# Kernel tuning notes

Hardware: AMD Instinct MI355X
Metric: run time of the kernel (lower is better)

The kernel has to match this reference:

```python
import jax, jax.numpy as jnp
import numpy as np

T, B, E, H = 2048, 2, 1024, 16
HD = E // H
NEG = -1e9  # large negative for causal additive mask


def setup_inputs() -> dict:
    key = jax.random.key(0)
    ks = jax.random.split(key, 6)
    s = 0.02
    query = jax.random.normal(ks[0], (T, B, E), jnp.float32)
    # causal additive mask, as commonly passed to this module's attn_mask arg
    attn_mask = jnp.triu(jnp.full((T, T), NEG, jnp.float32), k=1)
    key_padding_mask = jnp.zeros((B, T), jnp.bool_)
    Wq = jax.random.normal(ks[1], (E, E), jnp.float32) * s
    Wk = jax.random.normal(ks[2], (E, E), jnp.float32) * s
    Wv = jax.random.normal(ks[3], (E, E), jnp.float32) * s
    Wo = jax.random.normal(ks[4], (E, E), jnp.float32) * s
    bq = jnp.zeros((E,), jnp.float32)
    bk = jnp.zeros((E,), jnp.float32)
    bv = jnp.zeros((E,), jnp.float32)
    bo = jnp.zeros((E,), jnp.float32)
    return {"query": query, "attn_mask": attn_mask, "key_padding_mask": key_padding_mask,
            "Wq": Wq, "bq": bq, "Wk": Wk, "bk": bk, "Wv": Wv, "bv": bv, "Wo": Wo, "bo": bo}


def _shape(x):
    # [T, B, E] -> [B*H, T, HD]; E splits as (H, HD), flat index = b*H + h
    return x.reshape(T, B * H, HD).transpose(1, 0, 2)


def reference(query, attn_mask, key_padding_mask, Wq, bq, Wk, bk, Wv, bv, Wo, bo):
    scaling = HD ** -0.5
    q = (query @ Wq.T + bq) * scaling  # scale q as in torch code
    k = query @ Wk.T + bk              # self-attention path (static_kv=False)
    v = query @ Wv.T + bv
    q, k, v = _shape(q), _shape(k), _shape(v)            # [B*H, T, HD]
    w = jnp.einsum('bth,bsh->bts', q, k)                  # [B*H, T, S]
    w = w.reshape(B, H, T, T) + attn_mask                 # additive mask broadcast
    w = jnp.where(key_padding_mask[:, None, None, :], -jnp.inf, w)
    p = jax.nn.softmax(w, axis=-1).reshape(B * H, T, T)   # dropout p=0 (eval)
    o = jnp.einsum('bts,bsh->bth', p, v)                  # [B*H, T, HD]
    o = o.transpose(1, 0, 2).reshape(T, B, E)
    return o @ Wo.T + bo
```

## Files before the change

kernel.cpp:

```cpp
#include <hip/hip_runtime.h>

#define Tt 2048
#define Bb 2
#define Ee 1024
#define Hh 16
#define HD 64
#define BH 32

typedef __attribute__((ext_vector_type(8))) short short8;
typedef __attribute__((ext_vector_type(4))) short short4v;
typedef __attribute__((ext_vector_type(8))) __bf16 bf16x8;
typedef __attribute__((ext_vector_type(4))) float floatx4;

#define OFF_X  0
#define OFF_WQ 4194304
#define OFF_WK 5242880
#define OFF_WV 6291456
#define OFF_WO 7340032
#define OFF_Q  8388608
#define OFF_K  12582912
#define OFF_V  16777216
#define OFF_O  20971520

__device__ __forceinline__ short f2bf(float f) {
  union { float f; unsigned u; } a; a.f = f;
  unsigned r = a.u + 0x7fffu + ((a.u >> 16) & 1u);
  return (short)(r >> 16);
}

__device__ __forceinline__ floatx4 mfma16(short8 a, short8 b, floatx4 c) {
  return __builtin_amdgcn_mfma_f32_16x16x32_bf16(
      __builtin_bit_cast(bf16x8, a), __builtin_bit_cast(bf16x8, b), c, 0, 0, 0);
}

__device__ __forceinline__ floatx4 mfma_k16(short4v a, short4v b, floatx4 c) {
#if __has_builtin(__builtin_amdgcn_mfma_f32_16x16x16bf16_1k)
  return __builtin_amdgcn_mfma_f32_16x16x16bf16_1k(a, b, c, 0, 0, 0);
#else
  floatx4 d;
  asm("v_mfma_f32_16x16x16_bf16 %0, %1, %2, %3" : "=v"(d) : "v"(a), "v"(b), "v"(c));
  return d;
#endif
}

__device__ __forceinline__ void gl_lds16(const short* g, short* l) {
  __builtin_amdgcn_global_load_lds(
      (const __attribute__((address_space(1))) void*)g,
      (__attribute__((address_space(3))) void*)l, 16, 0, 0);
}

__global__ __launch_bounds__(256)
void convert_kernel(const float* __restrict__ x, const float* __restrict__ wq,
                    const float* __restrict__ wk, const float* __restrict__ wv,
                    const float* __restrict__ wo, short* __restrict__ dst)
{
  const int i4 = blockIdx.x * 256 + threadIdx.x;
  const int f = i4 * 4;
  const float* src;
  int local;
  if (f < 4194304) { src = x; local = f; }
  else {
    int gg = f - 4194304;
    int wsel = gg >> 20;
    local = gg & 1048575;
    src = (wsel == 0) ? wq : (wsel == 1) ? wk : (wsel == 2) ? wv : wo;
  }
  floatx4 v = *reinterpret_cast<const floatx4*>(src + local);
  short4 o;
  o.x = f2bf(v[0]); o.y = f2bf(v[1]); o.z = f2bf(v[2]); o.w = f2bf(v[3]);
  *reinterpret_cast<short4*>(dst + f) = o;
}

__global__ __launch_bounds__(256, 2)
void qkv_kernel(short* __restrict__ ws, const float* __restrict__ bq,
                const float* __restrict__ bk, const float* __restrict__ bv)
{
  __shared__ short smem[2][8192];
  const int t = threadIdx.x;
  const int lane = t & 63;
  const int w = t >> 6;
  const int g = lane >> 4, c = lane & 15;
  const int rb = blockIdx.x * 128;
  const int cb = blockIdx.y * 128;
  const int rw = (w >> 1) * 64, cw2 = (w & 1) * 64;

  const short* gA[2]; const short* gB[2]; int oC[2];
#pragma unroll
  for (int i = 0; i < 2; i++) {
    const int cid = t + 256 * i;
    const int row = cid >> 2;
    const int lch = (cid & 3) ^ ((row + (row >> 2)) & 3);
    gA[i] = ws + OFF_X + (rb + row) * 1024 + lch * 8;
    gB[i] = ws + OFF_WQ + (cb + row) * 1024 + lch * 8;
    oC[i] = cid * 8;
  }
  const int xr = (g ^ ((c + (c >> 2)) & 3)) * 8;

  floatx4 acc[4][4];
#pragma unroll
  for (int i = 0; i < 4; i++)
#pragma unroll
    for (int j = 0; j < 4; j++) acc[i][j] = (floatx4){0.f, 0.f, 0.f, 0.f};

#pragma unroll
  for (int i = 0; i < 2; i++) {
    gl_lds16(gA[i], &smem[0][oC[i]]);
    gl_lds16(gB[i], &smem[0][4096 + oC[i]]);
  }
  __syncthreads();

  for (int kt = 0; kt < 32; kt++) {
    const int cur = kt & 1;
    if (kt < 31) {
      const int kn = (kt + 1) * 32;
#pragma unroll
      for (int i = 0; i < 2; i++) {
        gl_lds16(gA[i] + kn, &smem[cur ^ 1][oC[i]]);
        gl_lds16(gB[i] + kn, &smem[cur ^ 1][4096 + oC[i]]);
      }
    }
    short8 af[4], bf[4];
#pragma unroll
    for (int mi = 0; mi < 4; mi++)
      af[mi] = *reinterpret_cast<const short8*>(&smem[cur][(rw + mi * 16 + c) * 32 + xr]);
#pragma unroll
    for (int ni = 0; ni < 4; ni++)
      bf[ni] = *reinterpret_cast<const short8*>(&smem[cur][4096 + (cw2 + ni * 16 + c) * 32 + xr]);
#pragma unroll
    for (int mi = 0; mi < 4; mi++)
#pragma unroll
      for (int ni = 0; ni < 4; ni++)
        acc[mi][ni] = mfma16(af[mi], bf[ni], acc[mi][ni]);
    __syncthreads();
  }

  const int m = cb >> 10;
  const int lcb = cb & 1023;
  if (m < 2) {
#pragma unroll
    for (int ni = 0; ni < 4; ni++) {
      const int lc = lcb + cw2 + ni * 16 + c;
      const int h = lc >> 6, d = lc & 63;
      const float bcol = (m == 0 ? bq : bk)[lc];
#pragma unroll
      for (int mi = 0; mi < 4; mi++)
#pragma unroll
        for (int r = 0; r < 4; r++) {
          const int row = rb + rw + mi * 16 + g * 4 + r;
          const int tt = row >> 1, b = row & 1;
          float v = acc[mi][ni][r] + bcol;
          if (m == 0) v *= 0.18033688f;
          ws[(m == 0 ? OFF_Q : OFF_K) + ((b * Hh + h) * Tt + tt) * HD + d] = f2bf(v);
        }
    }
  } else {
    short* vt = &smem[0][0];
    const int hb = lcb >> 6;
    for (int b = 0; b < 2; b++) {
      __syncthreads();
#pragma unroll
      for (int ni = 0; ni < 4; ni++) {
        const int lcol = cw2 + ni * 16 + c;
        const float bcol = bv[lcb + lcol];
#pragma unroll
        for (int mi = 0; mi < 4; mi++)
#pragma unroll
          for (int rr = 0; rr < 2; rr++) {
            const int r = rr * 2 + b;
            const int rloc = rw + mi * 16 + g * 4 + r;
            vt[lcol * 72 + (rloc >> 1)] = f2bf(acc[mi][ni][r] + bcol);
          }
      }
      __syncthreads();
#pragma unroll
      for (int i = 0; i < 4; i++) {
        const int u = t + 256 * i;
        const int lcol = u >> 3, seg = u & 7;
        short8 vv = *reinterpret_cast<const short8*>(vt + lcol * 72 + seg * 8);
        const int h = hb + (lcol >> 6), d = lcol & 63;
        *reinterpret_cast<short8*>(ws + OFF_V + ((b * Hh + h) * HD + d) * Tt
                                   + (rb >> 1) + seg * 8) = vv;
      }
    }
  }
}

__global__ __launch_bounds__(256, 2)
void gemm_o(const short* __restrict__ ws, const float* __restrict__ bo,
            float* __restrict__ dout)
{
  __shared__ short As[2][128 * 64];
  __shared__ short Bs[2][64 * 64];
  const int t = threadIdx.x;
  const int lane = t & 63;
  const int w = t >> 6;
  const int g = lane >> 4, c = lane & 15;
  const int rb = blockIdx.x * 128, cb = blockIdx.y * 64;
  const int rw = (w >> 1) * 64, cw = (w & 1) * 32;

  const short* gA[4]; int oA[4];
#pragma unroll
  for (int i = 0; i < 4; i++) {
    const int cid = t + 256 * i;
    const int row = cid >> 3;
    const int col8 = (cid & 7) ^ (row & 7);
    gA[i] = ws + OFF_O + (rb + row) * 1024 + col8 * 8;
    oA[i] = cid * 8;
  }
  const short* gB[2]; int oB[2];
#pragma unroll
  for (int i = 0; i < 2; i++) {
    const int cid = t + 256 * i;
    const int row = cid >> 3;
    const int col8 = (cid & 7) ^ (row & 7);
    gB[i] = ws + OFF_WO + (cb + row) * 1024 + col8 * 8;
    oB[i] = cid * 8;
  }
  const int x0 = (g ^ (c & 7)) * 8;

  floatx4 acc[4][2];
#pragma unroll
  for (int i = 0; i < 4; i++)
#pragma unroll
    for (int j = 0; j < 2; j++) acc[i][j] = (floatx4){0.f, 0.f, 0.f, 0.f};

#pragma unroll
  for (int i = 0; i < 4; i++) gl_lds16(gA[i], &As[0][oA[i]]);
#pragma unroll
  for (int i = 0; i < 2; i++) gl_lds16(gB[i], &Bs[0][oB[i]]);
  __syncthreads();

  for (int it = 0; it < 16; it++) {
    const int cur = it & 1;
    if (it < 15) {
      const int kn = (it + 1) * 64;
#pragma unroll
      for (int i = 0; i < 4; i++) gl_lds16(gA[i] + kn, &As[cur ^ 1][oA[i]]);
#pragma unroll
      for (int i = 0; i < 2; i++) gl_lds16(gB[i] + kn, &Bs[cur ^ 1][oB[i]]);
    }
#pragma unroll
    for (int kk = 0; kk < 2; kk++) {
      const int xo = x0 ^ (kk * 32);
      short8 af[4], bfr[2];
#pragma unroll
      for (int mi = 0; mi < 4; mi++)
        af[mi] = *reinterpret_cast<const short8*>(&As[cur][(rw + mi * 16 + c) * 64 + xo]);
#pragma unroll
      for (int ni = 0; ni < 2; ni++)
        bfr[ni] = *reinterpret_cast<const short8*>(&Bs[cur][(cw + ni * 16 + c) * 64 + xo]);
#pragma unroll
      for (int mi = 0; mi < 4; mi++)
#pragma unroll
        for (int ni = 0; ni < 2; ni++)
          acc[mi][ni] = mfma16(af[mi], bfr[ni], acc[mi][ni]);
    }
    __syncthreads();
  }

#pragma unroll
  for (int ni = 0; ni < 2; ni++) {
    const int col = cb + cw + ni * 16 + c;
    const float bcol = bo[col];
#pragma unroll
    for (int mi = 0; mi < 4; mi++)
#pragma unroll
      for (int r = 0; r < 4; r++) {
        const int row = rb + rw + mi * 16 + g * 4 + r;
        dout[row * 1024 + col] = acc[mi][ni][r] + bcol;
      }
  }
}

__global__ __launch_bounds__(256, 3)
void attn_kernel(short* __restrict__ ws, const unsigned char* __restrict__ kpm)
{
  __shared__ __align__(16) char smem[35840];
  short* KV  = reinterpret_cast<short*>(smem);
  float* bufA = reinterpret_cast<float*>(smem);
  float* bufB = reinterpret_cast<float*>(smem + 17408);
  float* Ls   = reinterpret_cast<float*>(smem + 34816);

  const int t = threadIdx.x;
  const int lane = t & 63;
  const int w = t >> 6;
  const int g = lane >> 4, c = lane & 15;
  const int bh = blockIdx.x;
  const int b = bh >> 4;
  const int h = bh & 15;
  const int qt = 31 - (int)blockIdx.y;
  const int qrow0 = qt * 64;

  const short* Qp = ws + OFF_Q + bh * Tt * HD;
  const short* Kp = ws + OFF_K + bh * Tt * HD;
  const short* Vp = ws + OFF_V + bh * HD * Tt;

  const short* gK[2]; const short* gV[2]; int lo[2];
#pragma unroll
  for (int i = 0; i < 2; i++) {
    const int cid = t + 256 * i;
    const int row = cid >> 3;
    const int col8 = (cid & 7) ^ (row & 7);
    gK[i] = Kp + row * HD + col8 * 8;
    gV[i] = Vp + row * Tt + col8 * 8;
    lo[i] = cid * 8;
  }

  short8 qf[4][2];
#pragma unroll
  for (int qs = 0; qs < 4; qs++) {
    const short* qr = Qp + (qrow0 + qs * 16 + c) * HD + g * 8;
    qf[qs][0] = *reinterpret_cast<const short8*>(qr);
    qf[qs][1] = *reinterpret_cast<const short8*>(qr + 32);
  }

  const uint4* kpv = reinterpret_cast<const uint4*>(kpm + b * Tt);
  uint4 k0v = kpv[lane * 2], k1v = kpv[lane * 2 + 1];
  const bool nz = (k0v.x | k0v.y | k0v.z | k0v.w | k1v.x | k1v.y | k1v.z | k1v.w) != 0;
  const unsigned long long kpany = __ballot(nz);

  float lt[4] = {0.f, 0.f, 0.f, 0.f};
  floatx4 acc[4][4];
#pragma unroll
  for (int i = 0; i < 4; i++)
#pragma unroll
    for (int j = 0; j < 4; j++) acc[i][j] = (floatx4){0.f, 0.f, 0.f, 0.f};

  const int ktmax = qt;
#pragma unroll
  for (int i = 0; i < 2; i++) gl_lds16(gK[i], &KV[lo[i]]);
#pragma unroll
  for (int i = 0; i < 2; i++) gl_lds16(gV[i], &KV[8192 + lo[i]]);
  __syncthreads();

  const int krow = w * 16 + c;
  const int kx0 = (g ^ (c & 7)) * 8;
  const int vcol = (((2 * w + (g >> 1)) ^ (c & 7)) * 8) + (g & 1) * 4;

  for (int kt = 0; kt <= ktmax; kt++) {
    const int cur = kt & 1;
    if (kt < ktmax) {
      const int kn = (kt + 1) * 64;
#pragma unroll
      for (int i = 0; i < 2; i++) gl_lds16(gK[i] + kn * HD, &KV[(cur ^ 1) * 4096 + lo[i]]);
#pragma unroll
      for (int i = 0; i < 2; i++) gl_lds16(gV[i] + kn, &KV[8192 + (cur ^ 1) * 4096 + lo[i]]);
    }
    const short* kr = &KV[cur * 4096 + krow * 64];
    const short8 kb0 = *reinterpret_cast<const short8*>(kr + kx0);
    const short8 kb1 = *reinterpret_cast<const short8*>(kr + (kx0 ^ 32));
    floatx4 st[4];
#pragma unroll
    for (int qs = 0; qs < 4; qs++) {
      floatx4 z = (floatx4){0.f, 0.f, 0.f, 0.f};
      z = mfma16(kb0, qf[qs][0], z);
      z = mfma16(kb1, qf[qs][1], z);
      st[qs] = z;
    }
    if ((kpany >> (2 * kt)) & 3ULL) {
#pragma unroll
      for (int r = 0; r < 4; r++)
        if (kpm[b * Tt + kt * 64 + w * 16 + g * 4 + r] != 0) {
#pragma unroll
          for (int qs = 0; qs < 4; qs++) st[qs][r] = -1e30f;
        }
    }
    if (kt == ktmax) {
      const int kl = w * 16 + g * 4;
#pragma unroll
      for (int qs = 0; qs < 4; qs++)
#pragma unroll
        for (int r = 0; r < 4; r++)
          if (kl + r > qs * 16 + c) st[qs][r] = -1e30f;
    }
    short4v pa[4];
#pragma unroll
    for (int qs = 0; qs < 4; qs++) {
      float p0 = __builtin_amdgcn_exp2f(st[qs][0]);
      float p1 = __builtin_amdgcn_exp2f(st[qs][1]);
      float p2 = __builtin_amdgcn_exp2f(st[qs][2]);
      float p3 = __builtin_amdgcn_exp2f(st[qs][3]);
      lt[qs] += (p0 + p1) + (p2 + p3);
      unsigned u0 = __builtin_bit_cast(unsigned, p0) + 0x8000u;
      unsigned u1 = __builtin_bit_cast(unsigned, p1) + 0x8000u;
      unsigned u2 = __builtin_bit_cast(unsigned, p2) + 0x8000u;
      unsigned u3 = __builtin_bit_cast(unsigned, p3) + 0x8000u;
      uint2 pk;
      pk.x = __builtin_amdgcn_perm(u1, u0, 0x07060302u);
      pk.y = __builtin_amdgcn_perm(u3, u2, 0x07060302u);
      pa[qs] = __builtin_bit_cast(short4v, pk);
    }
    const short* vb0 = &KV[8192 + cur * 4096];
    short4v vb[4];
#pragma unroll
    for (int dt = 0; dt < 4; dt++)
      vb[dt] = *reinterpret_cast<const short4v*>(vb0 + (dt * 16 + c) * 64 + vcol);
#pragma unroll
    for (int qs = 0; qs < 4; qs++)
#pragma unroll
      for (int dt = 0; dt < 4; dt++)
        acc[qs][dt] = mfma_k16(pa[qs], vb[dt], acc[qs][dt]);
    __syncthreads();
  }

#pragma unroll
  for (int qs = 0; qs < 4; qs++) {
    lt[qs] += __shfl_xor(lt[qs], 16);
    lt[qs] += __shfl_xor(lt[qs], 32);
  }
  if (g == 0) {
#pragma unroll
    for (int qs = 0; qs < 4; qs++) Ls[w * 64 + qs * 16 + c] = lt[qs];
  }
  float* mybuf = (w < 2) ? bufA : bufB;
  if ((w & 1) == 0) {
#pragma unroll
    for (int qs = 0; qs < 4; qs++)
#pragma unroll
      for (int dt = 0; dt < 4; dt++)
#pragma unroll
        for (int r = 0; r < 4; r++)
          mybuf[(qs * 16 + g * 4 + r) * 68 + dt * 16 + c] = acc[qs][dt][r];
  }
  __syncthreads();
  if (w & 1) {
#pragma unroll
    for (int qs = 0; qs < 4; qs++)
#pragma unroll
      for (int dt = 0; dt < 4; dt++)
#pragma unroll
        for (int r = 0; r < 4; r++)
          mybuf[(qs * 16 + g * 4 + r) * 68 + dt * 16 + c] += acc[qs][dt][r];
  }
  __syncthreads();
  const int row = w * 16 + (lane >> 2);
  const int dseg = (lane & 3) * 16;
  const float inv = 1.f / (Ls[row] + Ls[64 + row] + Ls[128 + row] + Ls[192 + row]);
  short* op = ws + OFF_O + ((qrow0 + row) * Bb + b) * Ee + h * 64 + dseg;
#pragma unroll
  for (int i = 0; i < 2; i++) {
    floatx4 a0 = *reinterpret_cast<const floatx4*>(&bufA[row * 68 + dseg + i * 8]);
    floatx4 a1 = *reinterpret_cast<const floatx4*>(&bufA[row * 68 + dseg + i * 8 + 4]);
    floatx4 b0 = *reinterpret_cast<const floatx4*>(&bufB[row * 68 + dseg + i * 8]);
    floatx4 b1 = *reinterpret_cast<const floatx4*>(&bufB[row * 68 + dseg + i * 8 + 4]);
    short8 s;
#pragma unroll
    for (int j = 0; j < 4; j++) s[j] = f2bf((a0[j] + b0[j]) * inv);
#pragma unroll
    for (int j = 0; j < 4; j++) s[4 + j] = f2bf((a1[j] + b1[j]) * inv);
    *reinterpret_cast<short8*>(op + i * 8) = s;
  }
}

extern "C" void kernel_launch(void* const* d_in, const int* in_sizes, int n_in,
                              void* d_out, int out_size, void* d_ws, size_t ws_size,
                              hipStream_t stream)
{
  const float* query = (const float*)d_in[0];
  const unsigned char* kpm = (const unsigned char*)d_in[2];
  const float* Wq = (const float*)d_in[3];
  const float* bq = (const float*)d_in[4];
  const float* Wk = (const float*)d_in[5];
  const float* bk = (const float*)d_in[6];
  const float* Wv = (const float*)d_in[7];
  const float* bv = (const float*)d_in[8];
  const float* Wo = (const float*)d_in[9];
  const float* bo = (const float*)d_in[10];
  short* ws = (short*)d_ws;
  float* out = (float*)d_out;

  convert_kernel<<<dim3(8192), dim3(256), 0, stream>>>(query, Wq, Wk, Wv, Wo, ws);
  qkv_kernel<<<dim3(32, 24), dim3(256), 0, stream>>>(ws, bq, bk, bv);
  attn_kernel<<<dim3(32, 32), dim3(256), 0, stream>>>(ws, kpm);
  gemm_o<<<dim3(32, 16), dim3(256), 0, stream>>>(ws, bo, out);
}
```

Before: 184.4 us.

## Drop LDS staging in attention, process key tiles in pairs, retile output GEMM

The attention kernel no longer stages K and V through LDS with double buffering. Each wave now reads its K and V fragments straight from global memory and handles two key tiles per iteration, so P·V can use the K=32 MFMA with its __syncthreads removed. The output projection GEMM moves to 128x128 tiles with a K-step of 32 and a new swizzle, and occupancy hints change. This removes LDS traffic and barriers but puts more load on global memory and the cache, and waves no longer share the K and V tiles they fetch.

Measured after the change: 206.0 us. 11.7% more time.

```diff
diff --git a/kernel.cpp b/kernel.cpp
--- a/kernel.cpp
+++ b/kernel.cpp
@@ -47,6 +47,22 @@
   __builtin_amdgcn_global_load_lds(
       (const __attribute__((address_space(1))) void*)g,
       (__attribute__((address_space(3))) void*)l, 16, 0, 0);
+}
+
+__device__ __forceinline__ uint2 exppack(floatx4 s, float& l) {
+  float p0 = __builtin_amdgcn_exp2f(s[0]);
+  float p1 = __builtin_amdgcn_exp2f(s[1]);
+  float p2 = __builtin_amdgcn_exp2f(s[2]);
+  float p3 = __builtin_amdgcn_exp2f(s[3]);
+  l += (p0 + p1) + (p2 + p3);
+  unsigned u0 = __builtin_bit_cast(unsigned, p0) + 0x8000u;
+  unsigned u1 = __builtin_bit_cast(unsigned, p1) + 0x8000u;
+  unsigned u2 = __builtin_bit_cast(unsigned, p2) + 0x8000u;
+  unsigned u3 = __builtin_bit_cast(unsigned, p3) + 0x8000u;
+  uint2 pk;
+  pk.x = __builtin_amdgcn_perm(u1, u0, 0x07060302u);
+  pk.y = __builtin_amdgcn_perm(u3, u2, 0x07060302u);
+  return pk;
 }
 
 __global__ __launch_bounds__(256)
@@ -189,78 +205,68 @@
 void gemm_o(const short* __restrict__ ws, const float* __restrict__ bo,
             float* __restrict__ dout)
 {
-  __shared__ short As[2][128 * 64];
-  __shared__ short Bs[2][64 * 64];
+  __shared__ short smem[2][8192];
   const int t = threadIdx.x;
   const int lane = t & 63;
   const int w = t >> 6;
   const int g = lane >> 4, c = lane & 15;
-  const int rb = blockIdx.x * 128, cb = blockIdx.y * 64;
-  const int rw = (w >> 1) * 64, cw = (w & 1) * 32;
-
-  const short* gA[4]; int oA[4];
-#pragma unroll
-  for (int i = 0; i < 4; i++) {
-    const int cid = t + 256 * i;
-    const int row = cid >> 3;
-    const int col8 = (cid & 7) ^ (row & 7);
-    gA[i] = ws + OFF_O + (rb + row) * 1024 + col8 * 8;
-    oA[i] = cid * 8;
-  }
-  const short* gB[2]; int oB[2];
+  const int rb = blockIdx.x * 128;
+  const int cb = blockIdx.y * 128;
+  const int rw = (w >> 1) * 64, cw2 = (w & 1) * 64;
+
+  const short* gA[2]; const short* gB[2]; int oC[2];
 #pragma unroll
   for (int i = 0; i < 2; i++) {
     const int cid = t + 256 * i;
-    const int row = cid >> 3;
-    const int col8 = (cid & 7) ^ (row & 7);
-    gB[i] = ws + OFF_WO + (cb + row) * 1024 + col8 * 8;
-    oB[i] = cid * 8;
-  }
-  const int x0 = (g ^ (c & 7)) * 8;
-
-  floatx4 acc[4][2];
+    const int row = cid >> 2;
+    const int lch = (cid & 3) ^ ((row + (row >> 2)) & 3);
+    gA[i] = ws + OFF_O + (rb + row) * 1024 + lch * 8;
+    gB[i] = ws + OFF_WO + (cb + row) * 1024 + lch * 8;
+    oC[i] = cid * 8;
+  }
+  const int xr = (g ^ ((c + (c >> 2)) & 3)) * 8;
+
+  floatx4 acc[4][4];
 #pragma unroll
   for (int i = 0; i < 4; i++)
 #pragma unroll
-    for (int j = 0; j < 2; j++) acc[i][j] = (floatx4){0.f, 0.f, 0.f, 0.f};
-
-#pragma unroll
-  for (int i = 0; i < 4; i++) gl_lds16(gA[i], &As[0][oA[i]]);
-#pragma unroll
-  for (int i = 0; i < 2; i++) gl_lds16(gB[i], &Bs[0][oB[i]]);
+    for (int j = 0; j < 4; j++) acc[i][j] = (floatx4){0.f, 0.f, 0.f, 0.f};
+
+#pragma unroll
+  for (int i = 0; i < 2; i++) {
+    gl_lds16(gA[i], &smem[0][oC[i]]);
+    gl_lds16(gB[i], &smem[0][4096 + oC[i]]);
+  }
   __syncthreads();
 
-  for (int it = 0; it < 16; it++) {
-    const int cur = it & 1;
-    if (it < 15) {
-      const int kn = (it + 1) * 64;
-#pragma unroll
-      for (int i = 0; i < 4; i++) gl_lds16(gA[i] + kn, &As[cur ^ 1][oA[i]]);
-#pragma unroll
-      for (int i = 0; i < 2; i++) gl_lds16(gB[i] + kn, &Bs[cur ^ 1][oB[i]]);
-    }
-#pragma unroll
-    for (int kk = 0; kk < 2; kk++) {
-      const int xo = x0 ^ (kk * 32);
-      short8 af[4], bfr[2];
-#pragma unroll
-      for (int mi = 0; mi < 4; mi++)
-        af[mi] = *reinterpret_cast<const short8*>(&As[cur][(rw + mi * 16 + c) * 64 + xo]);
-#pragma unroll
-      for (int ni = 0; ni < 2; ni++)
-        bfr[ni] = *reinterpret_cast<const short8*>(&Bs[cur][(cw + ni * 16 + c) * 64 + xo]);
-#pragma unroll
-      for (int mi = 0; mi < 4; mi++)
-#pragma unroll
-        for (int ni = 0; ni < 2; ni++)
-          acc[mi][ni] = mfma16(af[mi], bfr[ni], acc[mi][ni]);
-    }
+  for (int kt = 0; kt < 32; kt++) {
+    const int cur = kt & 1;
+    if (kt < 31) {
+      const int kn = (kt + 1) * 32;
+#pragma unroll
+      for (int i = 0; i < 2; i++) {
+        gl_lds16(gA[i] + kn, &smem[cur ^ 1][oC[i]]);
+        gl_lds16(gB[i] + kn, &smem[cur ^ 1][4096 + oC[i]]);
+      }
+    }
+    short8 af[4], bf[4];
+#pragma unroll
+    for (int mi = 0; mi < 4; mi++)
+      af[mi] = *reinterpret_cast<const short8*>(&smem[cur][(rw + mi * 16 + c) * 32 + xr]);
+#pragma unroll
+    for (int ni = 0; ni < 4; ni++)
+      bf[ni] = *reinterpret_cast<const short8*>(&smem[cur][4096 + (cw2 + ni * 16 + c) * 32 + xr]);
+#pragma unroll
+    for (int mi = 0; mi < 4; mi++)
+#pragma unroll
+      for (int ni = 0; ni < 4; ni++)
+        acc[mi][ni] = mfma16(af[mi], bf[ni], acc[mi][ni]);
     __syncthreads();
   }
 
 #pragma unroll
-  for (int ni = 0; ni < 2; ni++) {
-    const int col = cb + cw + ni * 16 + c;
+  for (int ni = 0; ni < 4; ni++) {
+    const int col = cb + cw2 + ni * 16 + c;
     const float bcol = bo[col];
 #pragma unroll
     for (int mi = 0; mi < 4; mi++)
@@ -272,11 +278,10 @@
   }
 }
 
-__global__ __launch_bounds__(256, 3)
+__global__ __launch_bounds__(256, 2)
 void attn_kernel(short* __restrict__ ws, const unsigned char* __restrict__ kpm)
 {
   __shared__ __align__(16) char smem[35840];
-  short* KV  = reinterpret_cast<short*>(smem);
   float* bufA = reinterpret_cast<float*>(smem);
   float* bufB = reinterpret_cast<float*>(smem + 17408);
   float* Ls   = reinterpret_cast<float*>(smem + 34816);
@@ -295,17 +300,6 @@
   const short* Kp = ws + OFF_K + bh * Tt * HD;
   const short* Vp = ws + OFF_V + bh * HD * Tt;
 
-  const short* gK[2]; const short* gV[2]; int lo[2];
-#pragma unroll
-  for (int i = 0; i < 2; i++) {
-    const int cid = t + 256 * i;
-    const int row = cid >> 3;
-    const int col8 = (cid & 7) ^ (row & 7);
-    gK[i] = Kp + row * HD + col8 * 8;
-    gV[i] = Vp + row * Tt + col8 * 8;
-    lo[i] = cid * 8;
-  }
-
   short8 qf[4][2];
 #pragma unroll
   for (int qs = 0; qs < 4; qs++) {
@@ -326,46 +320,113 @@
 #pragma unroll
     for (int j = 0; j < 4; j++) acc[i][j] = (floatx4){0.f, 0.f, 0.f, 0.f};
 
-  const int ktmax = qt;
-#pragma unroll
-  for (int i = 0; i < 2; i++) gl_lds16(gK[i], &KV[lo[i]]);
-#pragma unroll
-  for (int i = 0; i < 2; i++) gl_lds16(gV[i], &KV[8192 + lo[i]]);
-  __syncthreads();
-
-  const int krow = w * 16 + c;
-  const int kx0 = (g ^ (c & 7)) * 8;
-  const int vcol = (((2 * w + (g >> 1)) ^ (c & 7)) * 8) + (g & 1) * 4;
-
-  for (int kt = 0; kt <= ktmax; kt++) {
-    const int cur = kt & 1;
-    if (kt < ktmax) {
-      const int kn = (kt + 1) * 64;
-#pragma unroll
-      for (int i = 0; i < 2; i++) gl_lds16(gK[i] + kn * HD, &KV[(cur ^ 1) * 4096 + lo[i]]);
-#pragma unroll
-      for (int i = 0; i < 2; i++) gl_lds16(gV[i] + kn, &KV[8192 + (cur ^ 1) * 4096 + lo[i]]);
-    }
-    const short* kr = &KV[cur * 4096 + krow * 64];
-    const short8 kb0 = *reinterpret_cast<const short8*>(kr + kx0);
-    const short8 kb1 = *reinterpret_cast<const short8*>(kr + (kx0 ^ 32));
-    floatx4 st[4];
+  const short* Kw = Kp + (w * 16 + c) * HD + g * 8;
+  const short* Vl = Vp + c * Tt + w * 16 + g * 4;
+
+  const int NT = qt + 1, NP = NT >> 1, TAIL = NT & 1;
+
+  for (int pt = 0; pt < NP; pt++) {
+    const int ta = 2 * pt, tb = ta + 1;
+    const short* kap = Kw + ta * 4096;
+    const short* kbp = Kw + tb * 4096;
+    short8 kA0 = *reinterpret_cast<const short8*>(kap);
+    short8 kA1 = *reinterpret_cast<const short8*>(kap + 32);
+    short8 kB0 = *reinterpret_cast<const short8*>(kbp);
+    short8 kB1 = *reinterpret_cast<const short8*>(kbp + 32);
+    short4v vA[4], vB[4];
+#pragma unroll
+    for (int dt = 0; dt < 4; dt++) {
+      vA[dt] = *reinterpret_cast<const short4v*>(Vl + dt * 16 * Tt + ta * 64);
+      vB[dt] = *reinterpret_cast<const short4v*>(Vl + dt * 16 * Tt + tb * 64);
+    }
+    floatx4 sa[4], sb[4];
 #pragma unroll
     for (int qs = 0; qs < 4; qs++) {
       floatx4 z = (floatx4){0.f, 0.f, 0.f, 0.f};
-      z = mfma16(kb0, qf[qs][0], z);
-      z = mfma16(kb1, qf[qs][1], z);
+      z = mfma16(kA0, qf[qs][0], z);
+      z = mfma16(kA1, qf[qs][1], z);
+      sa[qs] = z;
+    }
+#pragma unroll
+    for (int qs = 0; qs < 4; qs++) {
+      floatx4 z = (floatx4){0.f, 0.f, 0.f, 0.f};
+      z = mfma16(kB0, qf[qs][0], z);
+      z = mfma16(kB1, qf[qs][1], z);
+      sb[qs] = z;
+    }
+    if ((kpany >> (2 * ta)) & 3ULL) {
+#pragma unroll
+      for (int r = 0; r < 4; r++)
+        if (kpm[b * Tt + ta * 64 + w * 16 + g * 4 + r] != 0) {
+#pragma unroll
+          for (int qs = 0; qs < 4; qs++) sa[qs][r] = -1e30f;
+        }
+    }
+    if ((kpany >> (2 * tb)) & 3ULL) {
+#pragma unroll
+      for (int r = 0; r < 4; r++)
+        if (kpm[b * Tt + tb * 64 + w * 16 + g * 4 + r] != 0) {
+#pragma unroll
+          for (int qs = 0; qs < 4; qs++) sb[qs][r] = -1e30f;
+        }
+    }
+    if (tb == qt) {
+      const int kl = w * 16 + g * 4;
+#pragma unroll
+      for (int qs = 0; qs < 4; qs++)
+#pragma unroll
+        for (int r = 0; r < 4; r++)
+          if (kl + r > qs * 16 + c) sb[qs][r] = -1e30f;
+    }
+    short8 pa8[4];
+#pragma unroll
+    for (int qs = 0; qs < 4; qs++) {
+      uint2 ua = exppack(sa[qs], lt[qs]);
+      uint2 ub = exppack(sb[qs], lt[qs]);
+      uint4 uu; uu.x = ua.x; uu.y = ua.y; uu.z = ub.x; uu.w = ub.y;
+      pa8[qs] = __builtin_bit_cast(short8, uu);
+    }
+    short8 vb8[4];
+#pragma unroll
+    for (int dt = 0; dt < 4; dt++) {
+      short8 vv;
+      vv[0] = vA[dt][0]; vv[1] = vA[dt][1]; vv[2] = vA[dt][2]; vv[3] = vA[dt][3];
+      vv[4] = vB[dt][0]; vv[5] = vB[dt][1]; vv[6] = vB[dt][2]; vv[7] = vB[dt][3];
+      vb8[dt] = vv;
+    }
+#pragma unroll
+    for (int qs = 0; qs < 4; qs++)
+#pragma unroll
+      for (int dt = 0; dt < 4; dt++)
+        acc[qs][dt] = mfma16(pa8[qs], vb8[dt], acc[qs][dt]);
+  }
+
+  if (TAIL) {
+    const int ta = NT - 1;
+    const short* kap = Kw + ta * 4096;
+    short8 kA0 = *reinterpret_cast<const short8*>(kap);
+    short8 kA1 = *reinterpret_cast<const short8*>(kap + 32);
+    short4v vA[4];
+#pragma unroll
+    for (int dt = 0; dt < 4; dt++)
+      vA[dt] = *reinterpret_cast<const short4v*>(Vl + dt * 16 * Tt + ta * 64);
+    floatx4 st[4];
+#pragma unroll
+    for (int qs = 0; qs < 4; qs++) {
+      floatx4 z = (floatx4){0.f, 0.f, 0.f, 0.f};
+      z = mfma16(kA0, qf[qs][0], z);
+      z = mfma16(kA1, qf[qs][1], z);
       st[qs] = z;
     }
-    if ((kpany >> (2 * kt)) & 3ULL) {
+    if ((kpany >> (2 * ta)) & 3ULL) {
 #pragma unroll
       for (int r = 0; r < 4; r++)
-        if (kpm[b * Tt + kt * 64 + w * 16 + g * 4 + r] != 0) {
+        if (kpm[b * Tt + ta * 64 + w * 16 + g * 4 + r] != 0) {
 #pragma unroll
           for (int qs = 0; qs < 4; qs++) st[qs][r] = -1e30f;
         }
     }
-    if (kt == ktmax) {
+    {
       const int kl = w * 16 + g * 4;
 #pragma unroll
       for (int qs = 0; qs < 4; qs++)
@@ -373,34 +434,17 @@
         for (int r = 0; r < 4; r++)
           if (kl + r > qs * 16 + c) st[qs][r] = -1e30f;
     }
-    short4v pa[4];
+    short4v pa4[4];
 #pragma unroll
     for (int qs = 0; qs < 4; qs++) {
-      float p0 = __builtin_amdgcn_exp2f(st[qs][0]);
-      float p1 = __builtin_amdgcn_exp2f(st[qs][1]);
-      float p2 = __builtin_amdgcn_exp2f(st[qs][2]);
-      float p3 = __builtin_amdgcn_exp2f(st[qs][3]);
-      lt[qs] += (p0 + p1) + (p2 + p3);
-      unsigned u0 = __builtin_bit_cast(unsigned, p0) + 0x8000u;
-      unsigned u1 = __builtin_bit_cast(unsigned, p1) + 0x8000u;
-      unsigned u2 = __builtin_bit_cast(unsigned, p2) + 0x8000u;
-      unsigned u3 = __builtin_bit_cast(unsigned, p3) + 0x8000u;
-      uint2 pk;
-      pk.x = __builtin_amdgcn_perm(u1, u0, 0x07060302u);
-      pk.y = __builtin_amdgcn_perm(u3, u2, 0x07060302u);
-      pa[qs] = __builtin_bit_cast(short4v, pk);
-    }
-    const short* vb0 = &KV[8192 + cur * 4096];
-    short4v vb[4];
-#pragma unroll
-    for (int dt = 0; dt < 4; dt++)
-      vb[dt] = *reinterpret_cast<const short4v*>(vb0 + (dt * 16 + c) * 64 + vcol);
+      uint2 u = exppack(st[qs], lt[qs]);
+      pa4[qs] = __builtin_bit_cast(short4v, u);
+    }
 #pragma unroll
     for (int qs = 0; qs < 4; qs++)
 #pragma unroll
       for (int dt = 0; dt < 4; dt++)
-        acc[qs][dt] = mfma_k16(pa[qs], vb[dt], acc[qs][dt]);
-    __syncthreads();
+        acc[qs][dt] = mfma_k16(pa4[qs], vA[dt], acc[qs][dt]);
   }
 
 #pragma unroll
@@ -472,5 +516,5 @@
   convert_kernel<<<dim3(8192), dim3(256), 0, stream>>>(query, Wq, Wk, Wv, Wo, ws);
   qkv_kernel<<<dim3(32, 24), dim3(256), 0, stream>>>(ws, bq, bk, bv);
   attn_kernel<<<dim3(32, 32), dim3(256), 0, stream>>>(ws, kpm);
-  gemm_o<<<dim3(32, 16), dim3(256), 0, stream>>>(ws, bo, out);
-}
+  gemm_o<<<dim3(32, 8), dim3(256), 0, stream>>>(ws, bo, out);
+}
```
